# Optimization experiments

Hardware: AMD Instinct MI355X
Metric: run time of the kernel (lower is better)

The kernel has to match this reference:

```python
import math
import jax, jax.numpy as jnp
from jax import lax
import numpy as np

KERNEL_SIZE = 25

def _gaussian_softmax_weights(k: int) -> jnp.ndarray:
    half = k // 2
    sigma = 1.0
    i = np.arange(k, dtype=np.float32)
    w = np.exp(-(((i - half) / (2.0 * sigma)) ** 2))
    w = np.exp(w - w.max())
    w = w / w.sum()
    return jnp.asarray(w, dtype=jnp.float32)  # [K]


def setup_inputs() -> dict:
    key = jax.random.key(0)
    x = jax.random.normal(key, (32, 2048, 512), dtype=jnp.float32)  # [B, L, C]
    w = _gaussian_softmax_weights(KERNEL_SIZE)                       # shared [K] kernel
    b = jnp.zeros((), dtype=jnp.float32)                             # scalar bias
    return {"x": x, "w": w, "b": b}


def reference(x, w, b):
    # x: [B, L, C]; w: [K]; b: scalar.
    # Original: per-channel conv1d with a single shared (1,1,K) kernel,
    # replicate padding. Fused here as one grouped depthwise conv.
    B, L, C = x.shape
    K = w.shape[0]
    p = K // 2
    xt = jnp.transpose(x, (0, 2, 1))                     # [B, C, L]
    xp = jnp.pad(xt, ((0, 0), (0, 0), (p, p)), mode="edge")  # replicate pad
    rhs = jnp.broadcast_to(w, (C, 1, K))                 # [O=C, I=1, K]
    out = lax.conv_general_dilated(
        xp, rhs,
        window_strides=(1,), padding="VALID",
        dimension_numbers=("NCH", "OIH", "NCH"),
        feature_group_count=C,
    )                                                    # [B, C, L]
    out = out + b
    return jnp.transpose(out, (0, 2, 1))                 # [B, L, C]
```

## Files before the change

kernel.cpp:

```cpp
#include <hip/hip_runtime.h>
#include <stdint.h>


typedef float f32x4 __attribute__((ext_vector_type(4)));

constexpr int K      = 25;
constexpr int HALF   = 12;
constexpr int BB     = 32;
constexpr int LL     = 2048;
constexpr int CC     = 512;
constexpr int TL     = 32;
constexpr int NROWS  = TL + K - 1;
constexpr int HC4    = 64;
constexpr int NTILE  = LL / TL;
constexpr int NBLK   = BB * NTILE * 2;

__device__ inline void gll16(const float* g, float* l) {
    __builtin_amdgcn_global_load_lds(
        (const __attribute__((address_space(1))) void*)g,
        (__attribute__((address_space(3))) void*)l, 16, 0, 0);
}

__global__ __launch_bounds__(256) void conv1d_dw_kernel(
    const float* __restrict__ x,
    const float* __restrict__ w,
    const float* __restrict__ bias_p,
    float* __restrict__ out)
{
    __shared__ float lds[NROWS * HC4 * 4];

    const int bid  = blockIdx.x;
    const int lbid = (bid & 7) * (NBLK >> 3) + (bid >> 3);

    const int ltile = lbid & (NTILE - 1);
    const int half  = (lbid >> 6) & 1;
    const int b     = lbid >> 7;

    const int tid  = threadIdx.x;
    const int wv   = tid >> 6;
    const int lane = tid & 63;

    const int l0 = ltile * TL;
    const size_t base = (size_t)b * LL * CC + (size_t)half * (HC4 * 4);

#pragma unroll
    for (int i = 0; i < NROWS / 4; ++i) {
        const int r    = wv * (NROWS / 4) + i;
        const int srcl = max(0, min(LL - 1, l0 - HALF + r));
        gll16(x + base + (size_t)srcl * CC + lane * 4, &lds[(r * HC4 + lane) * 4]);
    }

    float wr[K];
#pragma unroll
    for (int k = 0; k < K; ++k) wr[k] = w[k];
    const float bias = bias_p[0];

    __syncthreads();

    f32x4 acc[8];
#pragma unroll
    for (int j = 0; j < 8; ++j)
        acc[j] = (f32x4){bias, bias, bias, bias};

    const f32x4* ldsv = reinterpret_cast<const f32x4*>(lds);
#pragma unroll
    for (int rr = 0; rr < 32; ++rr) {
        const f32x4 v = ldsv[(wv * 8 + rr) * HC4 + lane];
#pragma unroll
        for (int j = 0; j < 8; ++j) {
            const int k = rr - j;
            if (k >= 0 && k < K) acc[j] += wr[k] * v;
        }
    }

    f32x4* ob = reinterpret_cast<f32x4*>(out + base) + (size_t)(l0 + wv * 8) * (CC / 4) + lane;
#pragma unroll
    for (int j = 0; j < 8; ++j)
        __builtin_nontemporal_store(acc[j], &ob[(size_t)j * (CC / 4)]);
}

extern "C" void kernel_launch(void* const* d_in, const int* in_sizes, int n_in,
                              void* d_out, int out_size, void* d_ws, size_t ws_size,
                              hipStream_t stream) {
    const float* x  = (const float*)d_in[0];
    const float* w  = (const float*)d_in[1];
    const float* bp = (const float*)d_in[2];
    float* out      = (float*)d_out;

    conv1d_dw_kernel<<<NBLK, 256, 0, stream>>>(x, w, bp, out);
}
```

Baseline: 48.14 us.

## Stream L-chunks through an LDS ring buffer with multi-stage async prefetch

Each block now covers 256 sequence positions over 128 channels, where before it covered 32 positions over 256 channels. Rows are staged into a 128-row LDS ring buffer with global_load_lds, three steps ahead of use, and explicit vmcnt waits and barriers overlap loading with compute. This cuts the halo reload overhead (24 extra rows per 32 outputs before) and hides memory latency, so HBM traffic drops. The cost is fewer blocks, per-step barriers, and narrower 128-channel rows, which may reduce coalescing.

```diff
diff --git a/kernel.cpp b/kernel.cpp
--- a/kernel.cpp
+++ b/kernel.cpp
@@ -1,5 +1,4 @@
 #include <hip/hip_runtime.h>
-#include <stdint.h>
 
 
 typedef float f32x4 __attribute__((ext_vector_type(4)));
@@ -9,11 +8,14 @@
 constexpr int BB     = 32;
 constexpr int LL     = 2048;
 constexpr int CC     = 512;
-constexpr int TL     = 32;
-constexpr int NROWS  = TL + K - 1;
-constexpr int HC4    = 64;
-constexpr int NTILE  = LL / TL;
-constexpr int NBLK   = BB * NTILE * 2;
+constexpr int QC     = 128;
+constexpr int STEP   = 32;
+constexpr int NSTEP  = 8;
+constexpr int LCHUNK = STEP * NSTEP;
+constexpr int NLCH   = LL / LCHUNK;
+constexpr int NQ     = CC / QC;
+constexpr int NBLK   = BB * NQ * NLCH;
+constexpr int RING   = 128;
 
 __device__ inline void gll16(const float* g, float* l) {
     __builtin_amdgcn_global_load_lds(
@@ -27,56 +29,78 @@
     const float* __restrict__ bias_p,
     float* __restrict__ out)
 {
-    __shared__ float lds[NROWS * HC4 * 4];
+    __shared__ float lds[RING * QC];
 
     const int bid  = blockIdx.x;
     const int lbid = (bid & 7) * (NBLK >> 3) + (bid >> 3);
 
-    const int ltile = lbid & (NTILE - 1);
-    const int half  = (lbid >> 6) & 1;
-    const int b     = lbid >> 7;
+    const int lch = lbid & (NLCH - 1);
+    const int q   = (lbid >> 3) & (NQ - 1);
+    const int b   = lbid >> 5;
 
     const int tid  = threadIdx.x;
     const int wv   = tid >> 6;
     const int lane = tid & 63;
+    const int lgrp = tid >> 5;
+    const int c4   = tid & 31;
 
-    const int l0 = ltile * TL;
-    const size_t base = (size_t)b * LL * CC + (size_t)half * (HC4 * 4);
-
-#pragma unroll
-    for (int i = 0; i < NROWS / 4; ++i) {
-        const int r    = wv * (NROWS / 4) + i;
-        const int srcl = max(0, min(LL - 1, l0 - HALF + r));
-        gll16(x + base + (size_t)srcl * CC + lane * 4, &lds[(r * HC4 + lane) * 4]);
-    }
+    const int Lbase = lch * LCHUNK;
+    const float* xq = x   + (size_t)b * LL * CC + q * QC;
+    float*       oq = out + (size_t)b * LL * CC + q * QC;
 
     float wr[K];
 #pragma unroll
     for (int k = 0; k < K; ++k) wr[k] = w[k];
     const float bias = bias_p[0];
 
-    __syncthreads();
+    auto stage = [&](int p) {
+#pragma unroll
+        for (int i = 0; i < 4; ++i) {
+            const int sbase = 8 * wv + 2 * i;
+            const int v0    = 32 * p + sbase;
+            const int s     = sbase + (lane >> 5);
+            const int li    = max(0, min(LL - 1, Lbase + 32 * p + s - 32));
+            gll16(xq + (size_t)li * CC + (lane & 31) * 4,
+                  lds + (size_t)(v0 & (RING - 1)) * QC);
+        }
+    };
 
-    f32x4 acc[8];
+    stage(0); stage(1); stage(2);
+
 #pragma unroll
-    for (int j = 0; j < 8; ++j)
-        acc[j] = (f32x4){bias, bias, bias, bias};
+    for (int t = 0; t < NSTEP; ++t) {
+        __builtin_amdgcn_s_barrier();
+        if (t < NSTEP - 1) {
+            stage(t + 3);
+            asm volatile("s_waitcnt vmcnt(4)" ::: "memory");
+        } else {
+            asm volatile("s_waitcnt vmcnt(0)" ::: "memory");
+        }
+        __builtin_amdgcn_s_barrier();
 
-    const f32x4* ldsv = reinterpret_cast<const f32x4*>(lds);
+        f32x4 acc[4];
 #pragma unroll
-    for (int rr = 0; rr < 32; ++rr) {
-        const f32x4 v = ldsv[(wv * 8 + rr) * HC4 + lane];
+        for (int jj = 0; jj < 4; ++jj) acc[jj] = (f32x4){bias, bias, bias, bias};
+
+        const int vb = 32 * t + lgrp * 4 + 20;
 #pragma unroll
-        for (int j = 0; j < 8; ++j) {
-            const int k = rr - j;
-            if (k >= 0 && k < K) acc[j] += wr[k] * v;
+        for (int rr = 0; rr < 28; ++rr) {
+            const int v = vb + rr;
+            const f32x4 rv = *reinterpret_cast<const f32x4*>(
+                lds + (size_t)(v & (RING - 1)) * QC + c4 * 4);
+#pragma unroll
+            for (int jj = 0; jj < 4; ++jj) {
+                const int k = rr - jj;
+                if (k >= 0 && k < K) acc[jj] += wr[k] * rv;
+            }
         }
+
+        const int l0 = Lbase + 32 * t + lgrp * 4;
+#pragma unroll
+        for (int jj = 0; jj < 4; ++jj)
+            __builtin_nontemporal_store(acc[jj],
+                reinterpret_cast<f32x4*>(oq + (size_t)(l0 + jj) * CC) + c4);
     }
-
-    f32x4* ob = reinterpret_cast<f32x4*>(out + base) + (size_t)(l0 + wv * 8) * (CC / 4) + lane;
-#pragma unroll
-    for (int j = 0; j < 8; ++j)
-        __builtin_nontemporal_store(acc[j], &ob[(size_t)j * (CC / 4)]);
 }
 
 extern "C" void kernel_launch(void* const* d_in, const int* in_sizes, int n_in,
```

New measurement: 49.15 us. 1.02x slower.

## Retile conv to 64-channel by 128-row tiles to cut halo reloads

Applied to the files above, without the earlier changes.

Each block now covers 64 channels and 128 sequence rows instead of 256 channels and 32 rows. Each 16-thread group computes 8 consecutive outputs for 4 channels. The halo of K-1 rows is amortized over more outputs, which reduces redundant global reads (1.19x instead of 1.75x). The cost is that each row's global load now touches only 256 bytes, which is narrower and may coalesce less well.

```diff
diff --git a/kernel.cpp b/kernel.cpp
--- a/kernel.cpp
+++ b/kernel.cpp
@@ -1,19 +1,21 @@
 #include <hip/hip_runtime.h>
-#include <stdint.h>
 
 
 typedef float f32x4 __attribute__((ext_vector_type(4)));
 
-constexpr int K      = 25;
-constexpr int HALF   = 12;
-constexpr int BB     = 32;
-constexpr int LL     = 2048;
-constexpr int CC     = 512;
-constexpr int TL     = 32;
-constexpr int NROWS  = TL + K - 1;
-constexpr int HC4    = 64;
-constexpr int NTILE  = LL / TL;
-constexpr int NBLK   = BB * NTILE * 2;
+constexpr int K     = 25;
+constexpr int HALF  = 12;
+constexpr int BB    = 32;
+constexpr int LL    = 2048;
+constexpr int CC    = 512;
+constexpr int QCH   = 64;
+constexpr int QC4   = QCH / 4;
+constexpr int TL    = 128;
+constexpr int NROWS = TL + K - 1;
+constexpr int NQUAD = NROWS / 4;
+constexpr int NQ    = CC / QCH;
+constexpr int NT    = LL / TL;
+constexpr int NBLK  = BB * NQ * NT;
 
 __device__ inline void gll16(const float* g, float* l) {
     __builtin_amdgcn_global_load_lds(
@@ -27,27 +29,32 @@
     const float* __restrict__ bias_p,
     float* __restrict__ out)
 {
-    __shared__ float lds[NROWS * HC4 * 4];
+    __shared__ float lds[NROWS * QCH];
 
     const int bid  = blockIdx.x;
     const int lbid = (bid & 7) * (NBLK >> 3) + (bid >> 3);
 
-    const int ltile = lbid & (NTILE - 1);
-    const int half  = (lbid >> 6) & 1;
-    const int b     = lbid >> 7;
+    const int lt = lbid & (NT - 1);
+    const int qc = (lbid >> 4) & (NQ - 1);
+    const int b  = lbid >> 7;
 
     const int tid  = threadIdx.x;
     const int wv   = tid >> 6;
     const int lane = tid & 63;
 
-    const int l0 = ltile * TL;
-    const size_t base = (size_t)b * LL * CC + (size_t)half * (HC4 * 4);
+    const int Lbase = lt * TL;
+    const float* xq = x   + (size_t)b * LL * CC + qc * QCH;
+    float*       oq = out + (size_t)b * LL * CC + qc * QCH;
 
 #pragma unroll
-    for (int i = 0; i < NROWS / 4; ++i) {
-        const int r    = wv * (NROWS / 4) + i;
-        const int srcl = max(0, min(LL - 1, l0 - HALF + r));
-        gll16(x + base + (size_t)srcl * CC + lane * 4, &lds[(r * HC4 + lane) * 4]);
+    for (int i = 0; i < 10; ++i) {
+        const int qd = wv + 4 * i;
+        if (qd < NQUAD) {
+            const int v  = qd * 4 + (lane >> 4);
+            const int li = max(0, min(LL - 1, Lbase + v - HALF));
+            gll16(xq + (size_t)li * CC + (lane & 15) * 4,
+                  lds + (size_t)qd * 4 * QCH);
+        }
     }
 
     float wr[K];
@@ -57,26 +64,29 @@
 
     __syncthreads();
 
+    const int lgrp = tid >> 4;
+    const int c4   = tid & 15;
+
     f32x4 acc[8];
 #pragma unroll
-    for (int j = 0; j < 8; ++j)
-        acc[j] = (f32x4){bias, bias, bias, bias};
+    for (int j = 0; j < 8; ++j) acc[j] = (f32x4){bias, bias, bias, bias};
 
     const f32x4* ldsv = reinterpret_cast<const f32x4*>(lds);
 #pragma unroll
     for (int rr = 0; rr < 32; ++rr) {
-        const f32x4 v = ldsv[(wv * 8 + rr) * HC4 + lane];
+        const f32x4 rv = ldsv[(size_t)(lgrp * 8 + rr) * QC4 + c4];
 #pragma unroll
         for (int j = 0; j < 8; ++j) {
             const int k = rr - j;
-            if (k >= 0 && k < K) acc[j] += wr[k] * v;
+            if (k >= 0 && k < K) acc[j] += wr[k] * rv;
         }
     }
 
-    f32x4* ob = reinterpret_cast<f32x4*>(out + base) + (size_t)(l0 + wv * 8) * (CC / 4) + lane;
+    const int l0 = Lbase + lgrp * 8;
 #pragma unroll
     for (int j = 0; j < 8; ++j)
-        __builtin_nontemporal_store(acc[j], &ob[(size_t)j * (CC / 4)]);
+        __builtin_nontemporal_store(acc[j],
+            reinterpret_cast<f32x4*>(oq + (size_t)(l0 + j) * CC) + c4);
 }
 
 extern "C" void kernel_launch(void* const* d_in, const int* in_sizes, int n_in,
```

Measured after the change: 43.61 us, median of 2. 1.1x faster.
